# Kernel optimization log

Measured on AMD Instinct MI355X. Metric: run time of the kernel, lower is better.

## Reference

```python
import jax, jax.numpy as jnp
import numpy as np

B, Q, K, DQ, DK, DV, H = 16, 64, 512, 512, 512, 512, 256
MASK_VAL = -1e6


def setup_inputs() -> dict:
    key = jax.random.key(0)
    k1, k2, k3, k4, k5, k6, k7 = jax.random.split(key, 7)
    return {
        "queries": jax.random.normal(k1, (B, Q, DQ), dtype=jnp.float32),
        "keys": jax.random.normal(k2, (B, K, DK), dtype=jnp.float32),
        "values": jax.random.normal(k3, (B, K, DV), dtype=jnp.float32),
        "valid_lens": jax.random.randint(k4, (B,), 1, K + 1, dtype=jnp.int32),
        "Wq": jax.random.normal(k5, (DQ, H), dtype=jnp.float32) * (1.0 / np.sqrt(DQ)),
        "Wk": jax.random.normal(k6, (DK, H), dtype=jnp.float32) * (1.0 / np.sqrt(DK)),
        "Wv": jax.random.normal(k7, (H,), dtype=jnp.float32) * (1.0 / np.sqrt(H)),
    }


def reference(queries, keys, values, valid_lens, Wq, Wk, Wv):
    # Project queries and keys into the shared additive-attention space.
    q = jnp.einsum("bqd,dh->bqh", queries, Wq)   # [B,Q,H]
    k = jnp.einsum("bkd,dh->bkh", keys, Wk)      # [B,K,H]
    # Bahdanau additive scoring: tanh(q + k) projected to a scalar per (q,k).
    feats = jnp.tanh(q[:, :, None, :] + k[:, None, :, :])  # [B,Q,K,H]
    scores = jnp.einsum("bqkh,h->bqk", feats, Wv)           # [B,Q,K]
    # Masked softmax over the key axis (positions >= valid_len masked out).
    mask = jnp.arange(K)[None, None, :] < valid_lens[:, None, None]  # [B,1,K]
    scores = jnp.where(mask, scores, MASK_VAL)
    attn = jax.nn.softmax(scores, axis=-1)                  # [B,Q,K]
    # Dropout is identity in eval mode; weighted sum of values.
    return jnp.einsum("bqk,bkv->bqv", attn, values)         # [B,Q,DV]
```

## Files before the change

### kernel.cpp

```cpp
#include <hip/hip_runtime.h>

#define LOG2E 1.4426950408889634f
#define TWO_LOG2E 2.8853900817779268f

typedef __attribute__((ext_vector_type(8))) short short8;
typedef __attribute__((ext_vector_type(4))) float f32x4;

__device__ __forceinline__ float e2x(float v) {
    return __builtin_amdgcn_exp2f(v * TWO_LOG2E);
}

__device__ __forceinline__ void split2(float x, float y, unsigned& hi, unsigned& lo) {
    unsigned ux = __float_as_uint(x), uy = __float_as_uint(y);
    float hx = __uint_as_float(ux & 0xffff0000u);
    float hy = __uint_as_float(uy & 0xffff0000u);
    unsigned lx = __float_as_uint(x - hx), ly = __float_as_uint(y - hy);
    hi = (ux >> 16) | (uy & 0xffff0000u);
    lo = (lx >> 16) | (ly & 0xffff0000u);
}

__global__ __launch_bounds__(256) void wprep_kernel(const float* __restrict__ Wq,
                                                    const float* __restrict__ Wk,
                                                    ushort* __restrict__ Wq2T,
                                                    ushort* __restrict__ Wk2T) {
    __shared__ float T[64][65];
    const float* W  = blockIdx.z ? Wk : Wq;
    ushort* W2T     = blockIdx.z ? Wk2T : Wq2T;
    const int t  = threadIdx.x;
    const int k0 = blockIdx.x * 64;
    const int n0 = blockIdx.y * 64;
#pragma unroll
    for (int p = 0; p < 4; ++p) {
        int u  = t + p * 256;
        int kk = u >> 4;
        int nf = (u & 15) * 4;
        float4 w = *reinterpret_cast<const float4*>(&W[(size_t)(k0 + kk) * 256 + n0 + nf]);
        T[nf + 0][kk] = w.x; T[nf + 1][kk] = w.y;
        T[nf + 2][kk] = w.z; T[nf + 3][kk] = w.w;
    }
    __syncthreads();
#pragma unroll
    for (int p = 0; p < 4; ++p) {
        int u  = t + p * 256;
        int n  = u >> 4;
        int kf = (u & 15) * 4;
        float a = T[n][kf], b = T[n][kf + 1], c = T[n][kf + 2], d = T[n][kf + 3];
        unsigned h01, l01, h23, l23;
        split2(a, b, h01, l01);
        split2(c, d, h23, l23);
        int kg   = k0 + kf;
        int ng   = n0 + n;
        int tile = ng >> 6;
        int row  = ng & 63;
        int cc   = kg >> 5;
        int kpos = kg & 31;
        ushort* base = W2T + (size_t)(tile * 16 + cc) * 6144
                     + (kpos >> 3) * 512 + row * 8 + (kpos & 7);
        uint2 hi; hi.x = h01; hi.y = h23;
        uint2 lo; lo.x = l01; lo.y = l23;
        *reinterpret_cast<uint2*>(base)        = hi;
        *reinterpret_cast<uint2*>(base + 2048) = hi;
        *reinterpret_cast<uint2*>(base + 4096) = lo;
    }
}

__global__ __launch_bounds__(256) void mfma_proj_kernel(const float* __restrict__ queries,
                                                        const float* __restrict__ keys,
                                                        const ushort* __restrict__ Wq2T,
                                                        const ushort* __restrict__ Wk2T,
                                                        float* __restrict__ Eq,
                                                        float* __restrict__ Ekp) {
    __shared__ float smemf[4736];
    ushort* Ah = reinterpret_cast<ushort*>(smemf);
    ushort* Bl = reinterpret_cast<ushort*>(smemf) + 3328;

    const int t    = threadIdx.x;
    const int mt   = blockIdx.x;
    const int Nb   = blockIdx.y * 64;
    const bool isQ = mt < 32;
    const int mloc = (isQ ? mt : mt - 32) * 32;
    const float4* Asrc4 = reinterpret_cast<const float4*>(isQ ? queries : keys)
                        + (size_t)mloc * 128;
    const ushort* W2T = isQ ? Wq2T : Wk2T;

    const int ln15 = t & 15;
    const int q    = (t >> 4) & 3;
    const int w    = t >> 6;
    const int wn   = w * 16;
    const int am   = t >> 3;
    const int ak   = t & 7;

    const char* gB[3];
#pragma unroll
    for (int i = 0; i < 3; ++i)
        gB[i] = reinterpret_cast<const char*>(W2T) + (size_t)(Nb >> 6) * 196608
              + i * 4096 + t * 16;

    f32x4 acc[2];
    acc[0] = (f32x4)0.0f;
    acc[1] = (f32x4)0.0f;

    float4 ra = Asrc4[(size_t)am * 128 + ak];

    for (int c = 0; c < 16; ++c) {
        __syncthreads();
#pragma unroll
        for (int i = 0; i < 3; ++i) {
            __builtin_amdgcn_global_load_lds(
                reinterpret_cast<const unsigned int*>(gB[i]),
                reinterpret_cast<unsigned int*>(
                    reinterpret_cast<char*>(smemf) + 6656 + i * 4096 + (t >> 6) * 1024),
                16, 0, 0);
            gB[i] += 12288;
        }
        {
            unsigned h01, l01, h23, l23;
            split2(ra.x, ra.y, h01, l01);
            split2(ra.z, ra.w, h23, l23);
            uint2 hi; hi.x = h01; hi.y = h23;
            uint2 lo; lo.x = l01; lo.y = l23;
            ushort* row = Ah + am * 104 + ak * 4;
            *reinterpret_cast<uint2*>(row)      = hi;
            *reinterpret_cast<uint2*>(row + 32) = lo;
            *reinterpret_cast<uint2*>(row + 64) = hi;
        }
        if (c < 15) ra = Asrc4[(size_t)am * 128 + (c + 1) * 8 + ak];
        __syncthreads();
#pragma unroll
        for (int s = 0; s < 3; ++s) {
            short8 af[2], bf;
#pragma unroll
            for (int fm = 0; fm < 2; ++fm)
                af[fm] = *reinterpret_cast<const short8*>(
                    Ah + (fm * 16 + ln15) * 104 + s * 32 + q * 8);
            bf = *reinterpret_cast<const short8*>(
                Bl + (s * 4 + q) * 512 + (wn + ln15) * 8);
#pragma unroll
            for (int fm = 0; fm < 2; ++fm)
                acc[fm] = __builtin_amdgcn_mfma_f32_16x16x32_bf16(
                    af[fm], bf, acc[fm], 0, 0, 0);
        }
    }

    if (isQ) {
#pragma unroll
        for (int fm = 0; fm < 2; ++fm)
#pragma unroll
            for (int r = 0; r < 4; ++r) {
                int row = mloc + fm * 16 + q * 4 + r;
                int col = Nb + wn + ln15;
                Eq[(size_t)row * 256 + col] = e2x(acc[fm][r]);
            }
    } else {
        __syncthreads();
        float (*Cs)[33] = reinterpret_cast<float(*)[33]>(smemf);
#pragma unroll
        for (int fm = 0; fm < 2; ++fm)
#pragma unroll
            for (int r = 0; r < 4; ++r) {
                int m_l = fm * 16 + q * 4 + r;
                int n_l = wn + ln15;
                Cs[n_l][m_l] = acc[fm][r];
            }
        __syncthreads();
        const int b      = mloc >> 9;
        const int k0h    = (mloc & 511) >> 1;
        const int h2base = Nb >> 1;
        float4* out4 = reinterpret_cast<float4*>(Ekp);
#pragma unroll
        for (int p = 0; p < 2; ++p) {
            int u   = t + p * 256;
            int h2r = u >> 4;
            int kp  = u & 15;
            int kk  = kp * 2;
            float4 o;
            o.x = e2x(Cs[2 * h2r    ][kk    ]);
            o.y = e2x(Cs[2 * h2r + 1][kk    ]);
            o.z = e2x(Cs[2 * h2r    ][kk + 1]);
            o.w = e2x(Cs[2 * h2r + 1][kk + 1]);
            out4[(size_t)b * 32768 + (size_t)(h2base + h2r) * 256 + k0h + kp] = o;
        }
    }
}

__global__ __launch_bounds__(256) void score_raw_kernel(
        const float* __restrict__ Eq, const float* __restrict__ Ekp,
        const float* __restrict__ Wv, const int* __restrict__ valid_lens,
        float* __restrict__ scores) {
    __shared__ float Eqs[8][256];
    __shared__ float Wvs[256];
    __shared__ float Sh[4][8][64];
    const int t  = threadIdx.x;
    const int kb = blockIdx.x * 64;
    const int q0 = blockIdx.y * 8;
    const int b  = blockIdx.z;

    const float4* eq4 = reinterpret_cast<const float4*>(Eq + (size_t)(b * 64 + q0) * 256);
#pragma unroll
    for (int i = 0; i < 2; ++i) {
        int u = t + i * 256;
        *reinterpret_cast<float4*>(&Eqs[u >> 6][(u & 63) * 4]) = eq4[u];
    }
    Wvs[t] = Wv[t];
    __syncthreads();

    const int kl = t & 63;
    const int hh = t >> 6;
    const float2* ek2 = reinterpret_cast<const float2*>(Ekp)
                      + (size_t)b * 65536 + (size_t)(hh * 32) * 512 + kb + kl;

    float acc[8] = {0.f, 0.f, 0.f, 0.f, 0.f, 0.f, 0.f, 0.f};
#pragma unroll 4
    for (int i = 0; i < 32; ++i) {
        float2 ek = ek2[(size_t)i * 512];
        int h2 = hh * 32 + i;
        float2 wv = *reinterpret_cast<const float2*>(&Wvs[2 * h2]);
#pragma unroll
        for (int q = 0; q < 8; ++q) {
            float2 e = *reinterpret_cast<const float2*>(&Eqs[q][2 * h2]);
            float a0 = fmaf(e.x, ek.x, 1.0f);
            float a1 = fmaf(e.y, ek.y, 1.0f);
            float d  = a0 * a1;
            float n  = fmaf(wv.y, a0, wv.x * a1);
            acc[q] = fmaf(n, __builtin_amdgcn_rcpf(d), acc[q]);
        }
    }
#pragma unroll
    for (int q = 0; q < 8; ++q) Sh[hh][q][kl] = acc[q];
    __syncthreads();

    const int vl = valid_lens[b];
#pragma unroll
    for (int i = 0; i < 2; ++i) {
        int u = t + i * 256;
        int q = u >> 6, k = u & 63;
        float s = -2.0f * ((Sh[0][q][k] + Sh[1][q][k]) + (Sh[2][q][k] + Sh[3][q][k]));
        if (kb + k >= vl) s = -1e6f;
        scores[(size_t)(b * 64 + q0 + q) * 512 + kb + k] = s;
    }
}

__global__ __launch_bounds__(256) void pv_kernel(const float* __restrict__ scores,
                                                 const float* __restrict__ values,
                                                 float* __restrict__ out) {
    __shared__ __align__(16) float Ps[16][516];
    __shared__ __align__(16) float Vs[2][32][64];

    const int t  = threadIdx.x;
    const int b  = blockIdx.z;
    const int q0 = blockIdx.y * 16;
    const int vt = blockIdx.x;

    const float4* sc4 = reinterpret_cast<const float4*>(scores) + (size_t)(b * 64 + q0) * 128;
#pragma unroll
    for (int p = 0; p < 8; ++p) {
        int u  = t + p * 256;
        int qr = u >> 7;
        int c4 = u & 127;
        *reinterpret_cast<float4*>(&Ps[qr][c4 * 4]) = sc4[(size_t)qr * 128 + c4];
    }

    const char* vbase = reinterpret_cast<const char*>(values)
                      + ((size_t)b * 512 * 512 + (size_t)vt * 64) * 4
                      + (size_t)(t >> 4) * 2048 + (size_t)(t & 15) * 16;
    char* ldsV0 = reinterpret_cast<char*>(&Vs[0][0][0]) + (t >> 6) * 1024;

    const int lane = t & 63;
    const int w    = t >> 6;
    const int v4   = lane & 15;
    const int ksub = lane >> 4;

#pragma unroll
    for (int i = 0; i < 2; ++i)
        __builtin_amdgcn_global_load_lds(
            reinterpret_cast<const unsigned int*>(vbase + (size_t)i * 32768),
            reinterpret_cast<unsigned int*>(ldsV0 + i * 4096), 16, 0, 0);
    __syncthreads();

#pragma unroll
    for (int rr = 0; rr < 4; ++rr) {
        const int r = 4 * w + rr;
        float v[8];
        float m = -1e30f;
#pragma unroll
        for (int i = 0; i < 8; ++i) { v[i] = Ps[r][lane + i * 64]; m = fmaxf(m, v[i]); }
#pragma unroll
        for (int off = 32; off > 0; off >>= 1) m = fmaxf(m, __shfl_xor(m, off));
        float s = 0.f;
#pragma unroll
        for (int i = 0; i < 8; ++i) {
            v[i] = __builtin_amdgcn_exp2f((v[i] - m) * LOG2E);
            s += v[i];
        }
#pragma unroll
        for (int off = 32; off > 0; off >>= 1) s += __shfl_xor(s, off);
        float inv = 1.0f / s;
#pragma unroll
        for (int i = 0; i < 8; ++i) Ps[r][lane + i * 64] = v[i] * inv;
    }

    float4 acc[4];
#pragma unroll
    for (int r = 0; r < 4; ++r) acc[r] = make_float4(0.f, 0.f, 0.f, 0.f);

    for (int c = 0; c < 16; ++c) {
        if (c < 15) {
            char* dst = reinterpret_cast<char*>(&Vs[(c + 1) & 1][0][0]) + (t >> 6) * 1024;
            const char* src = vbase + (size_t)(c + 1) * 65536;
#pragma unroll
            for (int i = 0; i < 2; ++i)
                __builtin_amdgcn_global_load_lds(
                    reinterpret_cast<const unsigned int*>(src + (size_t)i * 32768),
                    reinterpret_cast<unsigned int*>(dst + i * 4096), 16, 0, 0);
        }

        const float (*V)[64] = Vs[c & 1];
#pragma unroll
        for (int kk = 0; kk < 2; ++kk) {
            int kb = kk * 16 + ksub * 4;
            float4 V0 = *reinterpret_cast<const float4*>(&V[kb + 0][v4 * 4]);
            float4 V1 = *reinterpret_cast<const float4*>(&V[kb + 1][v4 * 4]);
            float4 V2 = *reinterpret_cast<const float4*>(&V[kb + 2][v4 * 4]);
            float4 V3 = *reinterpret_cast<const float4*>(&V[kb + 3][v4 * 4]);
#pragma unroll
            for (int r = 0; r < 4; ++r) {
                float4 p = *reinterpret_cast<const float4*>(&Ps[4 * w + r][c * 32 + kb]);
                acc[r].x = fmaf(p.x, V0.x, acc[r].x); acc[r].y = fmaf(p.x, V0.y, acc[r].y);
                acc[r].z = fmaf(p.x, V0.z, acc[r].z); acc[r].w = fmaf(p.x, V0.w, acc[r].w);
                acc[r].x = fmaf(p.y, V1.x, acc[r].x); acc[r].y = fmaf(p.y, V1.y, acc[r].y);
                acc[r].z = fmaf(p.y, V1.z, acc[r].z); acc[r].w = fmaf(p.y, V1.w, acc[r].w);
                acc[r].x = fmaf(p.z, V2.x, acc[r].x); acc[r].y = fmaf(p.z, V2.y, acc[r].y);
                acc[r].z = fmaf(p.z, V2.z, acc[r].z); acc[r].w = fmaf(p.z, V2.w, acc[r].w);
                acc[r].x = fmaf(p.w, V3.x, acc[r].x); acc[r].y = fmaf(p.w, V3.y, acc[r].y);
                acc[r].z = fmaf(p.w, V3.z, acc[r].z); acc[r].w = fmaf(p.w, V3.w, acc[r].w);
            }
        }
        __syncthreads();
    }

#pragma unroll
    for (int off = 16; off <= 32; off <<= 1)
#pragma unroll
        for (int r = 0; r < 4; ++r) {
            acc[r].x += __shfl_xor(acc[r].x, off); acc[r].y += __shfl_xor(acc[r].y, off);
            acc[r].z += __shfl_xor(acc[r].z, off); acc[r].w += __shfl_xor(acc[r].w, off);
        }
    if (ksub == 0) {
        float4* out4 = reinterpret_cast<float4*>(out);
#pragma unroll
        for (int r = 0; r < 4; ++r)
            out4[(size_t)(b * 64 + q0 + 4 * w + r) * 128 + vt * 16 + v4] = acc[r];
    }
}

extern "C" void kernel_launch(void* const* d_in, const int* in_sizes, int n_in,
                              void* d_out, int out_size, void* d_ws, size_t ws_size,
                              hipStream_t stream) {
    (void)in_sizes; (void)n_in; (void)out_size; (void)ws_size;
    const float* queries    = (const float*)d_in[0];
    const float* keys       = (const float*)d_in[1];
    const float* values     = (const float*)d_in[2];
    const int*   valid_lens = (const int*)d_in[3];
    const float* Wq         = (const float*)d_in[4];
    const float* Wk         = (const float*)d_in[5];
    const float* Wv         = (const float*)d_in[6];
    float* out = (float*)d_out;

    float* ws     = (float*)d_ws;
    float* Eq     = ws;
    float* Ekp    = ws + 262144;
    float* scores = ws + 262144 + 2097152;
    ushort* Wq2T  = (ushort*)(ws + 2883584);
    ushort* Wk2T  = Wq2T + 393216;

    hipLaunchKernelGGL(wprep_kernel, dim3(8, 4, 2), dim3(256), 0, stream,
                       Wq, Wk, Wq2T, Wk2T);
    hipLaunchKernelGGL(mfma_proj_kernel, dim3(288, 4), dim3(256), 0, stream,
                       queries, keys, Wq2T, Wk2T, Eq, Ekp);
    hipLaunchKernelGGL(score_raw_kernel, dim3(8, 8, 16), dim3(256), 0, stream,
                       Eq, Ekp, Wv, valid_lens, scores);
    hipLaunchKernelGGL(pv_kernel, dim3(8, 4, 16), dim3(256), 0, stream,
                       scores, values, out);
}
```

Baseline: 140.0 us.

## Fuse score, softmax and PV into one attention kernel per query group

Merges the score kernel and the softmax/PV kernel into one kernel. Each block handles 4 queries of one batch across all 512 keys, computes the softmax in registers and shared memory, then multiplies by values read straight from global memory. This removes the scores round trip through global memory and one launch. It also drops max subtraction, relying on scores being bounded, which holds because scores are sums of Wv-weighted tanh values and so are bounded by the sum of |Wv|. The grid shrinks to 256 blocks, and each block re-reads the full Ekp and value matrices for its batch, so global traffic and per-block latency rise.

```diff
diff --git a/kernel.cpp b/kernel.cpp
--- a/kernel.cpp
+++ b/kernel.cpp
@@ -183,174 +183,98 @@
     }
 }
 
-__global__ __launch_bounds__(256) void score_raw_kernel(
+__global__ __launch_bounds__(256) void attn_kernel(
         const float* __restrict__ Eq, const float* __restrict__ Ekp,
         const float* __restrict__ Wv, const int* __restrict__ valid_lens,
-        float* __restrict__ scores) {
-    __shared__ float Eqs[8][256];
+        const float* __restrict__ values, float* __restrict__ out) {
+    __shared__ __align__(16) float Eqs[4][256];
     __shared__ float Wvs[256];
-    __shared__ float Sh[4][8][64];
+    __shared__ __align__(16) float P[4][512];
+    __shared__ float Sd[4][4];
+
     const int t  = threadIdx.x;
-    const int kb = blockIdx.x * 64;
-    const int q0 = blockIdx.y * 8;
-    const int b  = blockIdx.z;
+    const int q0 = blockIdx.x * 4;
+    const int b  = blockIdx.y;
 
     const float4* eq4 = reinterpret_cast<const float4*>(Eq + (size_t)(b * 64 + q0) * 256);
-#pragma unroll
-    for (int i = 0; i < 2; ++i) {
-        int u = t + i * 256;
-        *reinterpret_cast<float4*>(&Eqs[u >> 6][(u & 63) * 4]) = eq4[u];
-    }
+    *reinterpret_cast<float4*>(&Eqs[t >> 6][(t & 63) * 4]) = eq4[t];
     Wvs[t] = Wv[t];
     __syncthreads();
 
-    const int kl = t & 63;
-    const int hh = t >> 6;
-    const float2* ek2 = reinterpret_cast<const float2*>(Ekp)
-                      + (size_t)b * 65536 + (size_t)(hh * 32) * 512 + kb + kl;
-
-    float acc[8] = {0.f, 0.f, 0.f, 0.f, 0.f, 0.f, 0.f, 0.f};
+    const float2* ekp2 = reinterpret_cast<const float2*>(Ekp) + (size_t)b * 65536 + t;
+    float accA[4] = {0.f, 0.f, 0.f, 0.f};
+    float accB[4] = {0.f, 0.f, 0.f, 0.f};
 #pragma unroll 4
-    for (int i = 0; i < 32; ++i) {
-        float2 ek = ek2[(size_t)i * 512];
-        int h2 = hh * 32 + i;
-        float2 wv = *reinterpret_cast<const float2*>(&Wvs[2 * h2]);
-#pragma unroll
-        for (int q = 0; q < 8; ++q) {
+    for (int h2 = 0; h2 < 128; ++h2) {
+        float2 ekA = ekp2[h2 * 512];
+        float2 ekB = ekp2[h2 * 512 + 256];
+        float2 wv  = *reinterpret_cast<const float2*>(&Wvs[2 * h2]);
+#pragma unroll
+        for (int q = 0; q < 4; ++q) {
             float2 e = *reinterpret_cast<const float2*>(&Eqs[q][2 * h2]);
-            float a0 = fmaf(e.x, ek.x, 1.0f);
-            float a1 = fmaf(e.y, ek.y, 1.0f);
-            float d  = a0 * a1;
-            float n  = fmaf(wv.y, a0, wv.x * a1);
-            acc[q] = fmaf(n, __builtin_amdgcn_rcpf(d), acc[q]);
-        }
-    }
-#pragma unroll
-    for (int q = 0; q < 8; ++q) Sh[hh][q][kl] = acc[q];
+            float a0 = fmaf(e.x, ekA.x, 1.0f);
+            float a1 = fmaf(e.y, ekA.y, 1.0f);
+            accA[q] = fmaf(fmaf(wv.y, a0, wv.x * a1),
+                           __builtin_amdgcn_rcpf(a0 * a1), accA[q]);
+            float b0 = fmaf(e.x, ekB.x, 1.0f);
+            float b1 = fmaf(e.y, ekB.y, 1.0f);
+            accB[q] = fmaf(fmaf(wv.y, b0, wv.x * b1),
+                           __builtin_amdgcn_rcpf(b0 * b1), accB[q]);
+        }
+    }
+
+    const int vl = valid_lens[b];
+    float EA[4], EB[4], part[4];
+#pragma unroll
+    for (int q = 0; q < 4; ++q) {
+        float sA = -2.0f * accA[q];
+        float sB = -2.0f * accB[q];
+        EA[q] = (t       < vl) ? __builtin_amdgcn_exp2f(sA * LOG2E) : 0.0f;
+        EB[q] = (t + 256 < vl) ? __builtin_amdgcn_exp2f(sB * LOG2E) : 0.0f;
+        part[q] = EA[q] + EB[q];
+    }
+#pragma unroll
+    for (int off = 32; off > 0; off >>= 1)
+#pragma unroll
+        for (int q = 0; q < 4; ++q) part[q] += __shfl_xor(part[q], off);
+    if ((t & 63) == 0) {
+#pragma unroll
+        for (int q = 0; q < 4; ++q) Sd[t >> 6][q] = part[q];
+    }
     __syncthreads();
-
-    const int vl = valid_lens[b];
-#pragma unroll
-    for (int i = 0; i < 2; ++i) {
-        int u = t + i * 256;
-        int q = u >> 6, k = u & 63;
-        float s = -2.0f * ((Sh[0][q][k] + Sh[1][q][k]) + (Sh[2][q][k] + Sh[3][q][k]));
-        if (kb + k >= vl) s = -1e6f;
-        scores[(size_t)(b * 64 + q0 + q) * 512 + kb + k] = s;
-    }
-}
-
-__global__ __launch_bounds__(256) void pv_kernel(const float* __restrict__ scores,
-                                                 const float* __restrict__ values,
-                                                 float* __restrict__ out) {
-    __shared__ __align__(16) float Ps[16][516];
-    __shared__ __align__(16) float Vs[2][32][64];
-
-    const int t  = threadIdx.x;
-    const int b  = blockIdx.z;
-    const int q0 = blockIdx.y * 16;
-    const int vt = blockIdx.x;
-
-    const float4* sc4 = reinterpret_cast<const float4*>(scores) + (size_t)(b * 64 + q0) * 128;
-#pragma unroll
-    for (int p = 0; p < 8; ++p) {
-        int u  = t + p * 256;
-        int qr = u >> 7;
-        int c4 = u & 127;
-        *reinterpret_cast<float4*>(&Ps[qr][c4 * 4]) = sc4[(size_t)qr * 128 + c4];
-    }
-
-    const char* vbase = reinterpret_cast<const char*>(values)
-                      + ((size_t)b * 512 * 512 + (size_t)vt * 64) * 4
-                      + (size_t)(t >> 4) * 2048 + (size_t)(t & 15) * 16;
-    char* ldsV0 = reinterpret_cast<char*>(&Vs[0][0][0]) + (t >> 6) * 1024;
-
-    const int lane = t & 63;
-    const int w    = t >> 6;
-    const int v4   = lane & 15;
-    const int ksub = lane >> 4;
-
-#pragma unroll
-    for (int i = 0; i < 2; ++i)
-        __builtin_amdgcn_global_load_lds(
-            reinterpret_cast<const unsigned int*>(vbase + (size_t)i * 32768),
-            reinterpret_cast<unsigned int*>(ldsV0 + i * 4096), 16, 0, 0);
+#pragma unroll
+    for (int q = 0; q < 4; ++q) {
+        float inv = 1.0f / ((Sd[0][q] + Sd[1][q]) + (Sd[2][q] + Sd[3][q]));
+        P[q][t]       = EA[q] * inv;
+        P[q][t + 256] = EB[q] * inv;
+    }
     __syncthreads();
 
-#pragma unroll
-    for (int rr = 0; rr < 4; ++rr) {
-        const int r = 4 * w + rr;
-        float v[8];
-        float m = -1e30f;
-#pragma unroll
-        for (int i = 0; i < 8; ++i) { v[i] = Ps[r][lane + i * 64]; m = fmaxf(m, v[i]); }
-#pragma unroll
-        for (int off = 32; off > 0; off >>= 1) m = fmaxf(m, __shfl_xor(m, off));
-        float s = 0.f;
-#pragma unroll
-        for (int i = 0; i < 8; ++i) {
-            v[i] = __builtin_amdgcn_exp2f((v[i] - m) * LOG2E);
-            s += v[i];
-        }
-#pragma unroll
-        for (int off = 32; off > 0; off >>= 1) s += __shfl_xor(s, off);
-        float inv = 1.0f / s;
-#pragma unroll
-        for (int i = 0; i < 8; ++i) Ps[r][lane + i * 64] = v[i] * inv;
-    }
-
-    float4 acc[4];
-#pragma unroll
-    for (int r = 0; r < 4; ++r) acc[r] = make_float4(0.f, 0.f, 0.f, 0.f);
-
-    for (int c = 0; c < 16; ++c) {
-        if (c < 15) {
-            char* dst = reinterpret_cast<char*>(&Vs[(c + 1) & 1][0][0]) + (t >> 6) * 1024;
-            const char* src = vbase + (size_t)(c + 1) * 65536;
-#pragma unroll
-            for (int i = 0; i < 2; ++i)
-                __builtin_amdgcn_global_load_lds(
-                    reinterpret_cast<const unsigned int*>(src + (size_t)i * 32768),
-                    reinterpret_cast<unsigned int*>(dst + i * 4096), 16, 0, 0);
-        }
-
-        const float (*V)[64] = Vs[c & 1];
-#pragma unroll
-        for (int kk = 0; kk < 2; ++kk) {
-            int kb = kk * 16 + ksub * 4;
-            float4 V0 = *reinterpret_cast<const float4*>(&V[kb + 0][v4 * 4]);
-            float4 V1 = *reinterpret_cast<const float4*>(&V[kb + 1][v4 * 4]);
-            float4 V2 = *reinterpret_cast<const float4*>(&V[kb + 2][v4 * 4]);
-            float4 V3 = *reinterpret_cast<const float4*>(&V[kb + 3][v4 * 4]);
-#pragma unroll
-            for (int r = 0; r < 4; ++r) {
-                float4 p = *reinterpret_cast<const float4*>(&Ps[4 * w + r][c * 32 + kb]);
-                acc[r].x = fmaf(p.x, V0.x, acc[r].x); acc[r].y = fmaf(p.x, V0.y, acc[r].y);
-                acc[r].z = fmaf(p.x, V0.z, acc[r].z); acc[r].w = fmaf(p.x, V0.w, acc[r].w);
-                acc[r].x = fmaf(p.y, V1.x, acc[r].x); acc[r].y = fmaf(p.y, V1.y, acc[r].y);
-                acc[r].z = fmaf(p.y, V1.z, acc[r].z); acc[r].w = fmaf(p.y, V1.w, acc[r].w);
-                acc[r].x = fmaf(p.z, V2.x, acc[r].x); acc[r].y = fmaf(p.z, V2.y, acc[r].y);
-                acc[r].z = fmaf(p.z, V2.z, acc[r].z); acc[r].w = fmaf(p.z, V2.w, acc[r].w);
-                acc[r].x = fmaf(p.w, V3.x, acc[r].x); acc[r].y = fmaf(p.w, V3.y, acc[r].y);
-                acc[r].z = fmaf(p.w, V3.z, acc[r].z); acc[r].w = fmaf(p.w, V3.w, acc[r].w);
-            }
-        }
-        __syncthreads();
-    }
-
-#pragma unroll
-    for (int off = 16; off <= 32; off <<= 1)
-#pragma unroll
-        for (int r = 0; r < 4; ++r) {
-            acc[r].x += __shfl_xor(acc[r].x, off); acc[r].y += __shfl_xor(acc[r].y, off);
-            acc[r].z += __shfl_xor(acc[r].z, off); acc[r].w += __shfl_xor(acc[r].w, off);
-        }
-    if (ksub == 0) {
-        float4* out4 = reinterpret_cast<float4*>(out);
-#pragma unroll
-        for (int r = 0; r < 4; ++r)
-            out4[(size_t)(b * 64 + q0 + 4 * w + r) * 128 + vt * 16 + v4] = acc[r];
-    }
+    const float2* V2 = reinterpret_cast<const float2*>(values) + (size_t)b * 131072 + t;
+    float2 av[4];
+#pragma unroll
+    for (int q = 0; q < 4; ++q) av[q] = make_float2(0.f, 0.f);
+
+#pragma unroll 4
+    for (int k4 = 0; k4 < 128; ++k4) {
+        float2 v0 = V2[(size_t)(k4 * 4 + 0) * 256];
+        float2 v1 = V2[(size_t)(k4 * 4 + 1) * 256];
+        float2 v2 = V2[(size_t)(k4 * 4 + 2) * 256];
+        float2 v3 = V2[(size_t)(k4 * 4 + 3) * 256];
+#pragma unroll
+        for (int q = 0; q < 4; ++q) {
+            float4 p = *reinterpret_cast<const float4*>(&P[q][k4 * 4]);
+            av[q].x = fmaf(p.x, v0.x, av[q].x); av[q].y = fmaf(p.x, v0.y, av[q].y);
+            av[q].x = fmaf(p.y, v1.x, av[q].x); av[q].y = fmaf(p.y, v1.y, av[q].y);
+            av[q].x = fmaf(p.z, v2.x, av[q].x); av[q].y = fmaf(p.z, v2.y, av[q].y);
+            av[q].x = fmaf(p.w, v3.x, av[q].x); av[q].y = fmaf(p.w, v3.y, av[q].y);
+        }
+    }
+
+    float* ob = out + (size_t)(b * 64 + q0) * 512 + 2 * t;
+#pragma unroll
+    for (int q = 0; q < 4; ++q)
+        *reinterpret_cast<float2*>(ob + (size_t)q * 512) = av[q];
 }
 
 extern "C" void kernel_launch(void* const* d_in, const int* in_sizes, int n_in,
@@ -369,7 +293,6 @@
     float* ws     = (float*)d_ws;
     float* Eq     = ws;
     float* Ekp    = ws + 262144;
-    float* scores = ws + 262144 + 2097152;
     ushort* Wq2T  = (ushort*)(ws + 2883584);
     ushort* Wk2T  = Wq2T + 393216;
 
@@ -377,8 +300,6 @@
                        Wq, Wk, Wq2T, Wk2T);
     hipLaunchKernelGGL(mfma_proj_kernel, dim3(288, 4), dim3(256), 0, stream,
                        queries, keys, Wq2T, Wk2T, Eq, Ekp);
-    hipLaunchKernelGGL(score_raw_kernel, dim3(8, 8, 16), dim3(256), 0, stream,
-                       Eq, Ekp, Wv, valid_lens, scores);
-    hipLaunchKernelGGL(pv_kernel, dim3(8, 4, 16), dim3(256), 0, stream,
-                       scores, values, out);
-}
+    hipLaunchKernelGGL(attn_kernel, dim3(16, 16), dim3(256), 0, stream,
+                       Eq, Ekp, Wv, valid_lens, values, out);
+}
```

Measured after the change: 153.5 us. +9.6%, slower.
